# Performance work log

Hardware: AMD Instinct MI355X
Metric: run time of the kernel (lower is better)

The kernel has to match this reference:

```python
import jax, jax.numpy as jnp
import numpy as np

MODEL_DIM = 1024
NUM_HEADS = 16
K_DIM = MODEL_DIM // NUM_HEADS


def setup_inputs() -> dict:
    key = jax.random.key(0)
    k1, k2, k3 = jax.random.split(key, 3)
    x = jax.random.normal(k1, (4, 2048, MODEL_DIM), dtype=jnp.float32)
    # nn.Linear(model_dim, 3*model_dim, bias=False): store as [D, 3D] so y = x @ W
    wqkv = jax.random.normal(k2, (MODEL_DIM, 3 * MODEL_DIM), dtype=jnp.float32) * (MODEL_DIM ** -0.5)
    wo = jax.random.normal(k3, (MODEL_DIM, MODEL_DIM), dtype=jnp.float32) * (MODEL_DIM ** -0.5)
    return {"x": x, "wqkv": wqkv, "wo": wo}


def reference(x, wqkv, wo):
    B, L, D = x.shape
    H, K = NUM_HEADS, K_DIM
    qkv = jnp.einsum("bld,de->ble", x, wqkv)  # [B, L, 3D]
    q, k, v = jnp.split(qkv, 3, axis=-1)
    # Faithful to source: plain reshape (no transpose) into [B, H, L, K]
    qh = q.reshape(B, H, L, K)
    kh = k.reshape(B, H, L, K)
    vh = v.reshape(B, H, L, K)
    scores = jnp.einsum("bhlk,bhmk->bhlm", qh, kh) / jnp.sqrt(jnp.float32(K))
    # Faithful quirk: softmax over dim=1 (head axis), as in the source
    probs = jax.nn.softmax(scores, axis=1)
    attended = jnp.einsum("bhlm,bhmk->bhlk", probs, vh)  # [B, H, L, K]
    concatted = attended.transpose(0, 2, 1, 3).reshape(B, L, D)
    return jnp.einsum("bld,de->ble", concatted, wo)
```

## Files before the change

### kernel.cpp

```cpp
#include <hip/hip_runtime.h>
#include <hip/hip_bf16.h>
#include <stdint.h>

typedef __attribute__((ext_vector_type(8))) short short8;
typedef __attribute__((ext_vector_type(4))) float floatx4;

#define QSCALE 0.18033688f

__device__ __forceinline__ unsigned short f2bf(float f) {
    unsigned int u = __float_as_uint(f);
    u += 0x7fffu + ((u >> 16) & 1u);
    return (unsigned short)(u >> 16);
}
__device__ __forceinline__ unsigned int pack2bf(float a, float b) {
    __hip_bfloat162 h = __float22bfloat162_rn(make_float2(a, b));
    return *reinterpret_cast<unsigned int*>(&h);
}

__device__ __forceinline__ void async16(const void* g, void* l) {
    __builtin_amdgcn_global_load_lds(
        (const __attribute__((address_space(1))) unsigned int*)g,
        (__attribute__((address_space(3))) unsigned int*)l, 16, 0, 0);
}

__global__ __launch_bounds__(256) void cvt_bf16(const float* __restrict__ src,
                                                unsigned short* __restrict__ dst, int n8) {
    int i = blockIdx.x * 256 + threadIdx.x;
    if (i >= n8) return;
    const float4 a = ((const float4*)src)[2 * i];
    const float4 b = ((const float4*)src)[2 * i + 1];
    ushort4 lo, hi;
    lo.x = f2bf(a.x); lo.y = f2bf(a.y); lo.z = f2bf(a.z); lo.w = f2bf(a.w);
    hi.x = f2bf(b.x); hi.y = f2bf(b.y); hi.z = f2bf(b.z); hi.w = f2bf(b.w);
    ((ushort4*)dst)[2 * i] = lo;
    ((ushort4*)dst)[2 * i + 1] = hi;
}

__global__ __launch_bounds__(256) void tcvt(const float* __restrict__ src,
                                            unsigned short* __restrict__ dst, int R, int C) {
    __shared__ unsigned short t[64][72];
    const int tid = threadIdx.x;
    const int r0 = blockIdx.y * 64, c0 = blockIdx.x * 64;
    #pragma unroll
    for (int it = 0; it < 4; it++) {
        int idx = it * 256 + tid;
        int rr = idx >> 4, cc = (idx & 15) * 4;
        float4 v = *(const float4*)(src + (size_t)(r0 + rr) * C + c0 + cc);
        t[cc + 0][rr] = f2bf(v.x);
        t[cc + 1][rr] = f2bf(v.y);
        t[cc + 2][rr] = f2bf(v.z);
        t[cc + 3][rr] = f2bf(v.w);
    }
    __syncthreads();
    #pragma unroll
    for (int it = 0; it < 2; it++) {
        int idx = it * 256 + tid;
        int cc = idx >> 3, r8 = (idx & 7) * 8;
        short8 v = *(const short8*)&t[cc][r8];
        *(short8*)(dst + (size_t)(c0 + cc) * R + r0 + r8) = v;
    }
}

__global__ __launch_bounds__(256) void vtrans(const unsigned short* __restrict__ vb,
                                              unsigned short* __restrict__ vbt) {
    __shared__ unsigned short t[64][72];
    const int tid = threadIdx.x;
    const int bh = blockIdx.y, m0 = blockIdx.x * 64;
    const unsigned short* src = vb + ((size_t)bh * 2048 + m0) * 64;
    unsigned short* dst = vbt + ((size_t)bh << 17) + m0;
    union { short8 v; unsigned short u[8]; } tmp;
    #pragma unroll
    for (int it = 0; it < 2; it++) {
        int idx = it * 256 + tid;
        int m = idx >> 3, c8 = (idx & 7) * 8;
        tmp.v = *(const short8*)(src + (size_t)m * 64 + c8);
        #pragma unroll
        for (int j = 0; j < 8; j++) t[c8 + j][m] = tmp.u[j];
    }
    __syncthreads();
    #pragma unroll
    for (int it = 0; it < 2; it++) {
        int idx = it * 256 + tid;
        int k = idx >> 3, c8 = (idx & 7) * 8;
        short8 v = *(const short8*)&t[k][c8];
        *(short8*)(dst + (size_t)k * 2048 + c8) = v;
    }
}

__global__ __launch_bounds__(256) void qkv_gemm(
    const unsigned short* __restrict__ A, const unsigned short* __restrict__ Bt,
    unsigned short* __restrict__ qb, unsigned short* __restrict__ kb,
    unsigned short* __restrict__ vb)
{
    __shared__ __align__(16) unsigned short As[128 * 32];
    __shared__ __align__(16) unsigned short Bs[128 * 32];
    const int tid = threadIdx.x, wave = tid >> 6, lane = tid & 63;
    const int quad = lane >> 4, lr = lane & 15;
    const int wr = wave >> 1, wc = wave & 1;
    const int bm = blockIdx.y * 128, bn = blockIdx.x * 128;
    const int lrow = lane >> 2, lcol = (lane & 3) * 8;

    floatx4 acc[4][4];
    #pragma unroll
    for (int i = 0; i < 4; i++)
        #pragma unroll
        for (int j = 0; j < 4; j++) acc[i][j] = (floatx4)0.0f;

    for (int k0 = 0; k0 < 1024; k0 += 32) {
        #pragma unroll
        for (int t = 0; t < 2; t++) {
            const int rbase = wave * 32 + t * 16;
            const int r = rbase + lrow;
            async16(A  + (size_t)(bm + r) * 1024 + k0 + lcol, &As[rbase * 32]);
            async16(Bt + (size_t)(bn + r) * 1024 + k0 + lcol, &Bs[rbase * 32]);
        }
        __syncthreads();
        short8 af[4], bfr[4];
        #pragma unroll
        for (int i = 0; i < 4; i++)
            af[i] = *(const short8*)&As[(wr * 64 + i * 16 + lr) * 32 + quad * 8];
        #pragma unroll
        for (int j = 0; j < 4; j++)
            bfr[j] = *(const short8*)&Bs[(wc * 64 + j * 16 + lr) * 32 + quad * 8];
        #pragma unroll
        for (int i = 0; i < 4; i++)
            #pragma unroll
            for (int j = 0; j < 4; j++)
                acc[i][j] = __builtin_amdgcn_mfma_f32_16x16x32_bf16(af[i], bfr[j], acc[i][j], 0, 0, 0);
        __syncthreads();
    }

    const int part = bn >> 10;
    unsigned short* __restrict__ dstb = (part == 0) ? qb : ((part == 1) ? kb : vb);
    const float sc = (part == 0) ? QSCALE : 1.0f;
    const int dbase = bn & 1023;
    #pragma unroll
    for (int i = 0; i < 4; i++)
        #pragma unroll
        for (int j = 0; j < 4; j++)
            #pragma unroll
            for (int r = 0; r < 4; r++) {
                int row = bm + wr * 64 + i * 16 + quad * 4 + r;
                int d   = dbase + wc * 64 + j * 16 + lr;
                int b = row >> 11, l = row & 2047;
                int flat = (l << 10) | d;
                int h = flat >> 17;
                int rem = flat & 131071;
                int l2 = rem >> 6, kk = rem & 63;
                dstb[((size_t)(b * 16 + h) * 2048 + l2) * 64 + kk] = f2bf(acc[i][j][r] * sc);
            }
}

__global__ __launch_bounds__(256) void out_gemm(
    const unsigned short* __restrict__ A, const unsigned short* __restrict__ Bt,
    float* __restrict__ C)
{
    __shared__ __align__(16) unsigned short As[128 * 32];
    __shared__ __align__(16) unsigned short Bs[128 * 32];
    const int tid = threadIdx.x, wave = tid >> 6, lane = tid & 63;
    const int quad = lane >> 4, lr = lane & 15;
    const int wr = wave >> 1, wc = wave & 1;
    const int bm = blockIdx.y * 128, bn = blockIdx.x * 128;
    const int lrow = lane >> 2, lcol = (lane & 3) * 8;

    floatx4 acc[4][4];
    #pragma unroll
    for (int i = 0; i < 4; i++)
        #pragma unroll
        for (int j = 0; j < 4; j++) acc[i][j] = (floatx4)0.0f;

    for (int k0 = 0; k0 < 1024; k0 += 32) {
        #pragma unroll
        for (int t = 0; t < 2; t++) {
            const int rbase = wave * 32 + t * 16;
            const int r = rbase + lrow;
            async16(A  + (size_t)(bm + r) * 1024 + k0 + lcol, &As[rbase * 32]);
            async16(Bt + (size_t)(bn + r) * 1024 + k0 + lcol, &Bs[rbase * 32]);
        }
        __syncthreads();
        short8 af[4], bfr[4];
        #pragma unroll
        for (int i = 0; i < 4; i++)
            af[i] = *(const short8*)&As[(wr * 64 + i * 16 + lr) * 32 + quad * 8];
        #pragma unroll
        for (int j = 0; j < 4; j++)
            bfr[j] = *(const short8*)&Bs[(wc * 64 + j * 16 + lr) * 32 + quad * 8];
        #pragma unroll
        for (int i = 0; i < 4; i++)
            #pragma unroll
            for (int j = 0; j < 4; j++)
                acc[i][j] = __builtin_amdgcn_mfma_f32_16x16x32_bf16(af[i], bfr[j], acc[i][j], 0, 0, 0);
        __syncthreads();
    }
    #pragma unroll
    for (int i = 0; i < 4; i++)
        #pragma unroll
        for (int j = 0; j < 4; j++)
            #pragma unroll
            for (int r = 0; r < 4; r++) {
                int row = bm + wr * 64 + i * 16 + quad * 4 + r;
                int col = bn + wc * 64 + j * 16 + lr;
                C[(size_t)row * 1024 + col] = acc[i][j][r];
            }
}

__global__ __launch_bounds__(256, 4) void attn_denom(
    const unsigned short* __restrict__ qb, const unsigned short* __restrict__ kb,
    unsigned short* __restrict__ drpT)
{
    __shared__ __align__(16) unsigned short Qs[64 * 64];
    __shared__ __align__(16) unsigned short Ks[64 * 64];
    const int tid = threadIdx.x, wave = tid >> 6, lane = tid & 63;
    const int quad = lane >> 4, lr = lane & 15;
    const int M0 = blockIdx.x * 64, L0 = blockIdx.y * 64, b = blockIdx.z;
    const int srow = tid >> 3, sblk = tid & 7;
    const int sphys = (sblk ^ (srow & 7)) * 8;

    floatx4 e[4];
    #pragma unroll
    for (int i = 0; i < 4; i++) e[i] = (floatx4)0.0f;

    {
        const size_t hb = ((size_t)(b * 16)) << 17;
        short8 q0 = *(const short8*)(qb + hb + (size_t)(L0 + srow) * 64 + sblk * 8);
        short8 q1 = *(const short8*)(qb + hb + (size_t)(L0 + srow + 32) * 64 + sblk * 8);
        short8 k0 = *(const short8*)(kb + hb + (size_t)(M0 + srow) * 64 + sblk * 8);
        short8 k1 = *(const short8*)(kb + hb + (size_t)(M0 + srow + 32) * 64 + sblk * 8);
        *(short8*)&Qs[srow * 64 + sphys] = q0;
        *(short8*)&Qs[(srow + 32) * 64 + sphys] = q1;
        *(short8*)&Ks[srow * 64 + sphys] = k0;
        *(short8*)&Ks[(srow + 32) * 64 + sphys] = k1;
    }
    __syncthreads();

    for (int h = 0; h < 16; h++) {
        short8 qn0, qn1, kn0, kn1;
        if (h < 15) {
            const size_t hb = ((size_t)(b * 16 + h + 1)) << 17;
            qn0 = *(const short8*)(qb + hb + (size_t)(L0 + srow) * 64 + sblk * 8);
            qn1 = *(const short8*)(qb + hb + (size_t)(L0 + srow + 32) * 64 + sblk * 8);
            kn0 = *(const short8*)(kb + hb + (size_t)(M0 + srow) * 64 + sblk * 8);
            kn1 = *(const short8*)(kb + hb + (size_t)(M0 + srow + 32) * 64 + sblk * 8);
        }
        const int rq = wave * 16 + lr;
        short8 qf0 = *(const short8*)&Qs[rq * 64 + ((quad) ^ (lr & 7)) * 8];
        short8 qf1 = *(const short8*)&Qs[rq * 64 + ((4 + quad) ^ (lr & 7)) * 8];
        #pragma unroll
        for (int mt = 0; mt < 4; mt++) {
            const int rk = mt * 16 + lr;
            short8 kf0 = *(const short8*)&Ks[rk * 64 + ((quad) ^ (lr & 7)) * 8];
            short8 kf1 = *(const short8*)&Ks[rk * 64 + ((4 + quad) ^ (lr & 7)) * 8];
            floatx4 s = (floatx4)0.0f;
            s = __builtin_amdgcn_mfma_f32_16x16x32_bf16(kf0, qf0, s, 0, 0, 0);
            s = __builtin_amdgcn_mfma_f32_16x16x32_bf16(kf1, qf1, s, 0, 0, 0);
            e[mt][0] += __builtin_amdgcn_exp2f(s[0]);
            e[mt][1] += __builtin_amdgcn_exp2f(s[1]);
            e[mt][2] += __builtin_amdgcn_exp2f(s[2]);
            e[mt][3] += __builtin_amdgcn_exp2f(s[3]);
        }
        __syncthreads();
        if (h < 15) {
            *(short8*)&Qs[srow * 64 + sphys] = qn0;
            *(short8*)&Qs[(srow + 32) * 64 + sphys] = qn1;
            *(short8*)&Ks[srow * 64 + sphys] = kn0;
            *(short8*)&Ks[(srow + 32) * 64 + sphys] = kn1;
            __syncthreads();
        }
    }
    #pragma unroll
    for (int mt = 0; mt < 4; mt++) {
        float r0 = __builtin_amdgcn_rcpf(e[mt][0]);
        float r1 = __builtin_amdgcn_rcpf(e[mt][1]);
        float r2 = __builtin_amdgcn_rcpf(e[mt][2]);
        float r3 = __builtin_amdgcn_rcpf(e[mt][3]);
        uint2 o;
        o.x = pack2bf(r0, r1);
        o.y = pack2bf(r2, r3);
        int mtg = (M0 >> 4) + mt;
        int ltg = (L0 >> 4) + wave;
        *(uint2*)(drpT + ((((size_t)b * 128 + mtg) * 128 + ltg) << 8) + lane * 4) = o;
    }
}

__global__ __launch_bounds__(256, 3) void attn_pv(
    const unsigned short* __restrict__ qb, const unsigned short* __restrict__ kb,
    const unsigned short* __restrict__ vbt, const unsigned short* __restrict__ drpT,
    unsigned short* __restrict__ cb)
{
    __shared__ __align__(16) unsigned short Ks[2][64 * 64];
    __shared__ __align__(16) unsigned short Vs[2][64 * 64];
    __shared__ __align__(16) unsigned short Ps[128 * 64];
    const int tid = threadIdx.x, wave = tid >> 6, lane = tid & 63;
    const int quad = lane >> 4, lr = lane & 15;
    const int e7 = lr & 7;
    const int flat = blockIdx.x;
    const int swz = (flat & 7) * 128 + (flat >> 3);
    const int Lt = swz & 15;
    const int h = (swz >> 4) & 15;
    const int b = swz >> 8;
    const int L0 = Lt * 128;
    const size_t head = (size_t)(b * 16 + h);
    const unsigned short* qbase = qb + (head << 17);
    const unsigned short* kbase = kb + (head << 17);
    const unsigned short* vtb   = vbt + (head << 17);
    const unsigned short* dbase = drpT + (((size_t)b * 128 * 128 + (L0 >> 4) + wave * 2) << 8) + lane * 4;

    const int klr = lane >> 3;
    const int ksw = (lane & 7) ^ klr;
    const unsigned short* ksrc0 = kbase + (size_t)(wave * 8 + klr) * 64 + ksw * 8;
    const unsigned short* vsrc0 = vtb + (size_t)(wave * 8 + klr) * 2048 + ksw * 8;

    short8 qf[2][2];
    #pragma unroll
    for (int j = 0; j < 2; j++) {
        const unsigned short* qr = qbase + (size_t)(L0 + wave * 32 + j * 16 + lr) * 64;
        qf[j][0] = *(const short8*)(qr + quad * 8);
        qf[j][1] = *(const short8*)(qr + 32 + quad * 8);
    }

    floatx4 oacc[2][4];
    #pragma unroll
    for (int i = 0; i < 2; i++)
        #pragma unroll
        for (int j = 0; j < 4; j++) oacc[i][j] = (floatx4)0.0f;

    async16(ksrc0,             &Ks[0][(wave * 8) * 64]);
    async16(ksrc0 + 32 * 64,   &Ks[0][(32 + wave * 8) * 64]);
    async16(vsrc0,             &Vs[0][(wave * 8) * 64]);
    async16(vsrc0 + 32 * 2048, &Vs[0][(32 + wave * 8) * 64]);
    uint2 du[4][2];
    #pragma unroll
    for (int mt = 0; mt < 4; mt++)
        #pragma unroll
        for (int j = 0; j < 2; j++)
            du[mt][j] = *(const uint2*)(dbase + ((size_t)mt << 15) + (j << 8));
    __syncthreads();

    for (int t = 0; t < 32; t++) {
        const int M0 = t * 64;
        const int cur = t & 1, nxt = cur ^ 1;
        if (t < 31) {
            const unsigned short* ks = ksrc0 + (size_t)(M0 + 64) * 64;
            const unsigned short* vs = vsrc0 + (M0 + 64);
            async16(ks,             &Ks[nxt][(wave * 8) * 64]);
            async16(ks + 32 * 64,   &Ks[nxt][(32 + wave * 8) * 64]);
            async16(vs,             &Vs[nxt][(wave * 8) * 64]);
            async16(vs + 32 * 2048, &Vs[nxt][(32 + wave * 8) * 64]);
        }
        const unsigned short* ksp = &Ks[cur][0];
        #pragma unroll
        for (int mt = 0; mt < 4; mt++) {
            const int rk = mt * 16 + lr;
            short8 kf0 = *(const short8*)&ksp[rk * 64 + (quad ^ e7) * 8];
            short8 kf1 = *(const short8*)&ksp[rk * 64 + ((4 + quad) ^ e7) * 8];
            #pragma unroll
            for (int j = 0; j < 2; j++) {
                uint2 duv = du[mt][j];
                floatx4 s = (floatx4)0.0f;
                __builtin_amdgcn_s_setprio(1);
                s = __builtin_amdgcn_mfma_f32_16x16x32_bf16(kf0, qf[j][0], s, 0, 0, 0);
                s = __builtin_amdgcn_mfma_f32_16x16x32_bf16(kf1, qf[j][1], s, 0, 0, 0);
                __builtin_amdgcn_s_setprio(0);
                float r0 = __uint_as_float(duv.x << 16);
                float r1 = __uint_as_float(duv.x & 0xffff0000u);
                float r2 = __uint_as_float(duv.y << 16);
                float r3 = __uint_as_float(duv.y & 0xffff0000u);
                float p0 = __builtin_amdgcn_exp2f(s[0]) * r0;
                float p1 = __builtin_amdgcn_exp2f(s[1]) * r1;
                float p2 = __builtin_amdgcn_exp2f(s[2]) * r2;
                float p3 = __builtin_amdgcn_exp2f(s[3]) * r3;
                uint2 o;
                o.x = pack2bf(p0, p1);
                o.y = pack2bf(p2, p3);
                const int l_loc = wave * 32 + j * 16 + lr;
                const int lb16 = mt * 2 + (quad >> 1);
                *(uint2*)&Ps[l_loc * 64 + (lb16 ^ e7) * 8 + (quad & 1) * 4] = o;
            }
        }
        if (t < 31) {
            #pragma unroll
            for (int mt = 0; mt < 4; mt++)
                #pragma unroll
                for (int j = 0; j < 2; j++)
                    du[mt][j] = *(const uint2*)(dbase + (((size_t)((t + 1) * 4 + mt)) << 15) + (j << 8));
        }
        __builtin_amdgcn_sched_barrier(0);
        const unsigned short* vsp = &Vs[cur][0];
        #pragma unroll
        for (int f = 0; f < 2; f++) {
            short8 pf[2], vf[4];
            #pragma unroll
            for (int i2 = 0; i2 < 2; i2++)
                pf[i2] = *(const short8*)&Ps[(wave * 32 + i2 * 16 + lr) * 64 + ((f * 4 + quad) ^ e7) * 8];
            #pragma unroll
            for (int j2 = 0; j2 < 4; j2++) {
                const int rv = j2 * 16 + lr;
                vf[j2] = *(const short8*)&vsp[rv * 64 + ((f * 4 + quad) ^ e7) * 8];
            }
            __builtin_amdgcn_s_setprio(1);
            #pragma unroll
            for (int j2 = 0; j2 < 4; j2++)
                #pragma unroll
                for (int i2 = 0; i2 < 2; i2++)
                    oacc[i2][j2] = __builtin_amdgcn_mfma_f32_16x16x32_bf16(
                        pf[i2], vf[j2], oacc[i2][j2], 0, 0, 0);
            __builtin_amdgcn_s_setprio(0);
        }
        if (t < 31) __syncthreads();
    }
    #pragma unroll
    for (int i2 = 0; i2 < 2; i2++)
        #pragma unroll
        for (int j2 = 0; j2 < 4; j2++)
            #pragma unroll
            for (int r = 0; r < 4; r++) {
                int row = L0 + wave * 32 + i2 * 16 + quad * 4 + r;
                int col = h * 64 + j2 * 16 + lr;
                cb[(size_t)(b * 2048 + row) * 1024 + col] = f2bf(oacc[i2][j2][r]);
            }
}

extern "C" void kernel_launch(void* const* d_in, const int* in_sizes, int n_in,
                              void* d_out, int out_size, void* d_ws, size_t ws_size,
                              hipStream_t stream) {
    const float* x    = (const float*)d_in[0];
    const float* wqkv = (const float*)d_in[1];
    const float* wo   = (const float*)d_in[2];
    float* out = (float*)d_out;

    unsigned short* W = (unsigned short*)d_ws;
    unsigned short* qb   = W;
    unsigned short* kb   = W + 8388608;
    unsigned short* vbt  = W + 16777216;
    unsigned short* drpT = W + 25165824;
    unsigned short* cb   = W + 41943040;
    unsigned short* xb    = drpT;
    unsigned short* wqkvT = drpT + 8388608;
    unsigned short* vb    = cb;
    unsigned short* woT   = drpT;

    cvt_bf16  <<<4096, 256, 0, stream>>>(x, xb, 1048576);
    tcvt      <<<dim3(48, 16), 256, 0, stream>>>(wqkv, wqkvT, 1024, 3072);
    qkv_gemm  <<<dim3(24, 64), 256, 0, stream>>>(xb, wqkvT, qb, kb, vb);
    vtrans    <<<dim3(32, 64), 256, 0, stream>>>(vb, vbt);
    attn_denom<<<dim3(32, 32, 4), 256, 0, stream>>>(qb, kb, drpT);
    attn_pv   <<<1024, 256, 0, stream>>>(qb, kb, vbt, drpT, cb);
    tcvt      <<<dim3(16, 16), 256, 0, stream>>>(wo, woT, 1024, 1024);
    out_gemm  <<<dim3(8, 64), 256, 0, stream>>>(cb, woT, out);
}
```

Measured before the change: 358.6 us.

## Double-buffer attn_denom with async LDS loads and hoist denominator prefetch in attn_pv

attn_denom now uses double-buffered Q/K tiles in LDS filled by global_load_lds async copies. This removes the register staging and one of the two barriers per head. Its launch bounds rise to 5 blocks per CU and MFMA sections get priority hints. attn_pv issues the next tile's denominator loads at the top of the iteration into a separate register set, so they overlap the whole iteration, at the cost of extra registers.

```diff
diff --git a/kernel.cpp b/kernel.cpp
--- a/kernel.cpp
+++ b/kernel.cpp
@@ -204,68 +204,64 @@
             }
 }
 
-__global__ __launch_bounds__(256, 4) void attn_denom(
+__global__ __launch_bounds__(256, 5) void attn_denom(
     const unsigned short* __restrict__ qb, const unsigned short* __restrict__ kb,
     unsigned short* __restrict__ drpT)
 {
-    __shared__ __align__(16) unsigned short Qs[64 * 64];
-    __shared__ __align__(16) unsigned short Ks[64 * 64];
+    __shared__ __align__(16) unsigned short Qs[2][64 * 64];
+    __shared__ __align__(16) unsigned short Ks[2][64 * 64];
     const int tid = threadIdx.x, wave = tid >> 6, lane = tid & 63;
     const int quad = lane >> 4, lr = lane & 15;
+    const int e7 = lr & 7;
     const int M0 = blockIdx.x * 64, L0 = blockIdx.y * 64, b = blockIdx.z;
-    const int srow = tid >> 3, sblk = tid & 7;
-    const int sphys = (sblk ^ (srow & 7)) * 8;
+
+    const int klr = lane >> 3;
+    const int ksw8 = ((lane & 7) ^ klr) * 8;
+    const size_t hb0 = ((size_t)(b * 16)) << 17;
+    const unsigned short* qsrc0 = qb + hb0 + (size_t)(L0 + wave * 8 + klr) * 64 + ksw8;
+    const unsigned short* ksrc0 = kb + hb0 + (size_t)(M0 + wave * 8 + klr) * 64 + ksw8;
 
     floatx4 e[4];
     #pragma unroll
     for (int i = 0; i < 4; i++) e[i] = (floatx4)0.0f;
 
-    {
-        const size_t hb = ((size_t)(b * 16)) << 17;
-        short8 q0 = *(const short8*)(qb + hb + (size_t)(L0 + srow) * 64 + sblk * 8);
-        short8 q1 = *(const short8*)(qb + hb + (size_t)(L0 + srow + 32) * 64 + sblk * 8);
-        short8 k0 = *(const short8*)(kb + hb + (size_t)(M0 + srow) * 64 + sblk * 8);
-        short8 k1 = *(const short8*)(kb + hb + (size_t)(M0 + srow + 32) * 64 + sblk * 8);
-        *(short8*)&Qs[srow * 64 + sphys] = q0;
-        *(short8*)&Qs[(srow + 32) * 64 + sphys] = q1;
-        *(short8*)&Ks[srow * 64 + sphys] = k0;
-        *(short8*)&Ks[(srow + 32) * 64 + sphys] = k1;
-    }
+    async16(qsrc0,           &Qs[0][(wave * 8) * 64]);
+    async16(qsrc0 + 32 * 64, &Qs[0][(32 + wave * 8) * 64]);
+    async16(ksrc0,           &Ks[0][(wave * 8) * 64]);
+    async16(ksrc0 + 32 * 64, &Ks[0][(32 + wave * 8) * 64]);
     __syncthreads();
 
     for (int h = 0; h < 16; h++) {
-        short8 qn0, qn1, kn0, kn1;
+        const int cur = h & 1, nxt = cur ^ 1;
         if (h < 15) {
-            const size_t hb = ((size_t)(b * 16 + h + 1)) << 17;
-            qn0 = *(const short8*)(qb + hb + (size_t)(L0 + srow) * 64 + sblk * 8);
-            qn1 = *(const short8*)(qb + hb + (size_t)(L0 + srow + 32) * 64 + sblk * 8);
-            kn0 = *(const short8*)(kb + hb + (size_t)(M0 + srow) * 64 + sblk * 8);
-            kn1 = *(const short8*)(kb + hb + (size_t)(M0 + srow + 32) * 64 + sblk * 8);
-        }
+            const unsigned short* qs = qsrc0 + ((size_t)(h + 1) << 17);
+            const unsigned short* ks = ksrc0 + ((size_t)(h + 1) << 17);
+            async16(qs,           &Qs[nxt][(wave * 8) * 64]);
+            async16(qs + 32 * 64, &Qs[nxt][(32 + wave * 8) * 64]);
+            async16(ks,           &Ks[nxt][(wave * 8) * 64]);
+            async16(ks + 32 * 64, &Ks[nxt][(32 + wave * 8) * 64]);
+        }
+        const unsigned short* qsp = &Qs[cur][0];
+        const unsigned short* ksp = &Ks[cur][0];
         const int rq = wave * 16 + lr;
-        short8 qf0 = *(const short8*)&Qs[rq * 64 + ((quad) ^ (lr & 7)) * 8];
-        short8 qf1 = *(const short8*)&Qs[rq * 64 + ((4 + quad) ^ (lr & 7)) * 8];
+        short8 qf0 = *(const short8*)&qsp[rq * 64 + (quad ^ e7) * 8];
+        short8 qf1 = *(const short8*)&qsp[rq * 64 + ((4 + quad) ^ e7) * 8];
         #pragma unroll
         for (int mt = 0; mt < 4; mt++) {
             const int rk = mt * 16 + lr;
-            short8 kf0 = *(const short8*)&Ks[rk * 64 + ((quad) ^ (lr & 7)) * 8];
-            short8 kf1 = *(const short8*)&Ks[rk * 64 + ((4 + quad) ^ (lr & 7)) * 8];
+            short8 kf0 = *(const short8*)&ksp[rk * 64 + (quad ^ e7) * 8];
+            short8 kf1 = *(const short8*)&ksp[rk * 64 + ((4 + quad) ^ e7) * 8];
             floatx4 s = (floatx4)0.0f;
+            __builtin_amdgcn_s_setprio(1);
             s = __builtin_amdgcn_mfma_f32_16x16x32_bf16(kf0, qf0, s, 0, 0, 0);
             s = __builtin_amdgcn_mfma_f32_16x16x32_bf16(kf1, qf1, s, 0, 0, 0);
+            __builtin_amdgcn_s_setprio(0);
             e[mt][0] += __builtin_amdgcn_exp2f(s[0]);
             e[mt][1] += __builtin_amdgcn_exp2f(s[1]);
             e[mt][2] += __builtin_amdgcn_exp2f(s[2]);
             e[mt][3] += __builtin_amdgcn_exp2f(s[3]);
         }
-        __syncthreads();
-        if (h < 15) {
-            *(short8*)&Qs[srow * 64 + sphys] = qn0;
-            *(short8*)&Qs[(srow + 32) * 64 + sphys] = qn1;
-            *(short8*)&Ks[srow * 64 + sphys] = kn0;
-            *(short8*)&Ks[(srow + 32) * 64 + sphys] = kn1;
-            __syncthreads();
-        }
+        if (h < 15) __syncthreads();
     }
     #pragma unroll
     for (int mt = 0; mt < 4; mt++) {
@@ -339,6 +335,7 @@
     for (int t = 0; t < 32; t++) {
         const int M0 = t * 64;
         const int cur = t & 1, nxt = cur ^ 1;
+        uint2 dun[4][2];
         if (t < 31) {
             const unsigned short* ks = ksrc0 + (size_t)(M0 + 64) * 64;
             const unsigned short* vs = vsrc0 + (M0 + 64);
@@ -346,7 +343,13 @@
             async16(ks + 32 * 64,   &Ks[nxt][(32 + wave * 8) * 64]);
             async16(vs,             &Vs[nxt][(wave * 8) * 64]);
             async16(vs + 32 * 2048, &Vs[nxt][(32 + wave * 8) * 64]);
-        }
+            #pragma unroll
+            for (int mt = 0; mt < 4; mt++)
+                #pragma unroll
+                for (int j = 0; j < 2; j++)
+                    dun[mt][j] = *(const uint2*)(dbase + (((size_t)((t + 1) * 4 + mt)) << 15) + (j << 8));
+        }
+        __builtin_amdgcn_sched_barrier(0);
         const unsigned short* ksp = &Ks[cur][0];
         #pragma unroll
         for (int mt = 0; mt < 4; mt++) {
@@ -377,14 +380,6 @@
                 *(uint2*)&Ps[l_loc * 64 + (lb16 ^ e7) * 8 + (quad & 1) * 4] = o;
             }
         }
-        if (t < 31) {
-            #pragma unroll
-            for (int mt = 0; mt < 4; mt++)
-                #pragma unroll
-                for (int j = 0; j < 2; j++)
-                    du[mt][j] = *(const uint2*)(dbase + (((size_t)((t + 1) * 4 + mt)) << 15) + (j << 8));
-        }
-        __builtin_amdgcn_sched_barrier(0);
         const unsigned short* vsp = &Vs[cur][0];
         #pragma unroll
         for (int f = 0; f < 2; f++) {
@@ -406,7 +401,14 @@
                         pf[i2], vf[j2], oacc[i2][j2], 0, 0, 0);
             __builtin_amdgcn_s_setprio(0);
         }
-        if (t < 31) __syncthreads();
+        if (t < 31) {
+            #pragma unroll
+            for (int mt = 0; mt < 4; mt++)
+                #pragma unroll
+                for (int j = 0; j < 2; j++)
+                    du[mt][j] = dun[mt][j];
+            __syncthreads();
+        }
     }
     #pragma unroll
     for (int i2 = 0; i2 < 2; i2++)
```

Result: slower. 370.4 us (+3.3%).
